# Kernel optimization log

Hardware: AMD Instinct MI355X
Metric: run time of the kernel (lower is better)

## Reference

```python
import jax, jax.numpy as jnp
import numpy as np

HIDDEN = 256
HEADS = 8
HEAD_DIM = HIDDEN // HEADS
SCALE = HEAD_DIM ** -0.5
N = 4096
NUM_GRAPHS = 16
LN_EPS = 1e-5


def setup_inputs() -> dict:
    key = jax.random.key(0)
    ks = jax.random.split(key, 8)
    x = jax.random.normal(ks[0], (N, HIDDEN), dtype=jnp.float32)
    batch = jnp.sort(jax.random.randint(ks[1], (N,), 0, NUM_GRAPHS, dtype=jnp.int64))
    # Xavier-uniform linear weights, stored as [in, out] (y = x @ W + b)
    lim = float(np.sqrt(6.0 / (HIDDEN + HIDDEN)))
    def W(k):
        return jax.random.uniform(k, (HIDDEN, HIDDEN), jnp.float32, -lim, lim)
    return {
        "x": x,
        "batch": batch,
        "Wq": W(ks[2]), "bq": jnp.zeros((HIDDEN,), jnp.float32),
        "Wk": W(ks[3]), "bk": jnp.zeros((HIDDEN,), jnp.float32),
        "Wv": W(ks[4]), "bv": jnp.zeros((HIDDEN,), jnp.float32),
        "Wo": W(ks[5]), "bo": jnp.zeros((HIDDEN,), jnp.float32),
        "gamma": jnp.ones((HIDDEN,), jnp.float32),
        "beta": jnp.zeros((HIDDEN,), jnp.float32),
    }


def _layer_norm(x, gamma, beta):
    mu = jnp.mean(x, axis=-1, keepdims=True)
    var = jnp.mean(jnp.square(x - mu), axis=-1, keepdims=True)
    return (x - mu) * jax.lax.rsqrt(var + LN_EPS) * gamma + beta


def reference(x, batch, Wq, bq, Wk, bk, Wv, bv, Wo, bo, gamma, beta):
    residual = x
    h = _layer_norm(x, gamma, beta)
    n = h.shape[0]
    q = (h @ Wq + bq).reshape(n, HEADS, HEAD_DIM)
    k = (h @ Wk + bk).reshape(n, HEADS, HEAD_DIM)
    v = (h @ Wv + bv).reshape(n, HEADS, HEAD_DIM)
    # dense scores masked to block-diagonal (same-graph) structure
    scores = jnp.einsum('ihd,jhd->ihj', q, k) * SCALE  # [N, H, N]
    same_graph = (batch[None, :] == batch[:, None])[:, None, :]  # [N, 1, N]
    scores = jnp.where(same_graph, scores, -jnp.inf)
    attn = jax.nn.softmax(scores, axis=-1)
    attn = jnp.nan_to_num(attn, nan=0.0)
    out = jnp.einsum('ihj,jhd->ihd', attn, v).reshape(n, HIDDEN)
    out = out @ Wo + bo
    return residual + out
```

## Files before the change

### kernel.cpp

```cpp
#include <hip/hip_runtime.h>

#define NNODES 4096
#define HID 256
#define NG 16
#define NH 8
#define HD 32
#define LN_EPS 1e-5f
#define QSCALE (0.17677669529663687f * 1.4426950408889634f)
#define CAPT 384
#define VTS (CAPT + 2)

typedef unsigned short u16;
typedef unsigned int u32;
typedef __bf16 bf16x8 __attribute__((ext_vector_type(8)));
typedef float f32x4 __attribute__((ext_vector_type(4)));

__device__ __forceinline__ float bf2f(u16 u){
  union { u32 i; float f; } c; c.i = ((u32)u) << 16; return c.f;
}
__device__ __forceinline__ u16 f2bf(float f){
  union { float f; u32 i; } c; c.f = f;
  u32 x = c.i;
  return (u16)((x + 0x7fffu + ((x >> 16) & 1u)) >> 16);
}

__global__ __launch_bounds__(256) void prep_kernel(
    const float* __restrict__ x, const float* __restrict__ gamma,
    const float* __restrict__ beta, u16* __restrict__ h,
    const float* __restrict__ Wq, const float* __restrict__ Wk,
    const float* __restrict__ Wv, const float* __restrict__ Wo,
    u16* __restrict__ Wt, const int* __restrict__ bw, int* __restrict__ seg){
  __shared__ u16 tile[32][33];
  __shared__ int bad;
  int b = blockIdx.x;
  if (b < 1024){
    int wave = threadIdx.x >> 6, lane = threadIdx.x & 63;
    int row = b * 4 + wave;
    float4 xv = ((const float4*)x)[row * 64 + lane];
    float a0 = xv.x, a1 = xv.y, a2 = xv.z, a3 = xv.w;
    float s = a0 + a1 + a2 + a3;
    #pragma unroll
    for (int m = 1; m < 64; m <<= 1) s += __shfl_xor(s, m);
    float mu = s * (1.0f / HID);
    float d0 = a0 - mu, d1 = a1 - mu, d2 = a2 - mu, d3 = a3 - mu;
    float vv = d0*d0 + d1*d1 + d2*d2 + d3*d3;
    #pragma unroll
    for (int m = 1; m < 64; m <<= 1) vv += __shfl_xor(vv, m);
    float rs = rsqrtf(vv * (1.0f / HID) + LN_EPS);
    float4 gv = ((const float4*)gamma)[lane];
    float4 bv = ((const float4*)beta)[lane];
    ushort4 o;
    o.x = f2bf(d0 * rs * gv.x + bv.x);
    o.y = f2bf(d1 * rs * gv.y + bv.y);
    o.z = f2bf(d2 * rs * gv.z + bv.z);
    o.w = f2bf(d3 * rs * gv.w + bv.w);
    *(ushort4*)(h + (size_t)row * HID + lane * 4) = o;
  } else if (b < 1280){
    int idx = b - 1024;
    int w = idx >> 6;
    int t = idx & 63;
    int bx = (t & 7) * 32, by = (t >> 3) * 32;
    const float* src = (w == 0) ? Wq : (w == 1) ? Wk : (w == 2) ? Wv : Wo;
    u16* dst = Wt + (size_t)w * HID * HID;
    int tx = threadIdx.x & 31, ty = threadIdx.x >> 5;
    #pragma unroll
    for (int r = 0; r < 32; r += 8)
      tile[ty + r][tx] = f2bf(src[(size_t)(by + ty + r) * HID + bx + tx]);
    __syncthreads();
    #pragma unroll
    for (int r = 0; r < 32; r += 8)
      dst[(size_t)(bx + ty + r) * HID + by + tx] = tile[tx][ty + r];
  } else {
    if (threadIdx.x == 0) bad = 0;
    __syncthreads();
    int local_bad = 0;
    for (int i = threadIdx.x; i < NNODES; i += 256){
      int v = bw[i];
      if (v < 0 || v > 15) local_bad = 1;
      if (i + 1 < NNODES && bw[i + 1] < v) local_bad = 1;
    }
    if (local_bad) atomicOr(&bad, 1);
    __syncthreads();
    int stride = bad ? 2 : 1;
    int g = threadIdx.x;
    if (g <= NG){
      int lo = 0, hi = NNODES;
      while (lo < hi){
        int mid = (lo + hi) >> 1;
        if (bw[mid * stride] < g) lo = mid + 1; else hi = mid;
      }
      seg[g] = lo;
    }
  }
}

template<bool FINAL>
__device__ __forceinline__ void gemm_tile(const u16* __restrict__ A, const u16* __restrict__ Bt,
    const float* __restrict__ bias, const float* __restrict__ resid, void* __restrict__ out){
  int gw = blockIdx.x * 4 + (threadIdx.x >> 6);
  int lane = threadIdx.x & 63;
  int lr = lane & 15, lq = lane >> 4;
  int m0 = (gw >> 4) * 64;
  int n0 = (gw & 15) * 16;
  f32x4 acc[4] = {};
  const u16* arow = A + (size_t)(m0 + lr) * HID + lq * 8;
  const u16* brow = Bt + (size_t)(n0 + lr) * HID + lq * 8;
  #pragma unroll
  for (int k0 = 0; k0 < HID; k0 += 32){
    bf16x8 b = *(const bf16x8*)(brow + k0);
    #pragma unroll
    for (int t = 0; t < 4; t++){
      bf16x8 a = *(const bf16x8*)(arow + (size_t)t * 16 * HID + k0);
      acc[t] = __builtin_amdgcn_mfma_f32_16x16x32_bf16(a, b, acc[t], 0, 0, 0);
    }
  }
  int col = n0 + lr;
  float bb = bias[col];
  #pragma unroll
  for (int t = 0; t < 4; t++){
    #pragma unroll
    for (int r = 0; r < 4; r++){
      int row = m0 + 16 * t + lq * 4 + r;
      float val = acc[t][r] + bb;
      if (FINAL){
        val += resid[(size_t)row * HID + col];
        ((float*)out)[(size_t)row * HID + col] = val;
      } else {
        ((u16*)out)[(size_t)row * HID + col] = f2bf(val);
      }
    }
  }
}

__global__ __launch_bounds__(256) void gemm_qkv_kernel(const u16* __restrict__ h,
    const u16* __restrict__ Wt, const float* __restrict__ bq, const float* __restrict__ bk,
    const float* __restrict__ bv, u16* __restrict__ q, u16* __restrict__ k, u16* __restrict__ v){
  int which = blockIdx.y;
  const u16* B = Wt + (size_t)which * HID * HID;
  const float* bias = (which == 0) ? bq : (which == 1) ? bk : bv;
  u16* out = (which == 0) ? q : (which == 1) ? k : v;
  gemm_tile<false>(h, B, bias, nullptr, out);
}

__global__ __launch_bounds__(256) void gemm_proj_kernel(const u16* __restrict__ ao,
    const u16* __restrict__ WtO, const float* __restrict__ bo, const float* __restrict__ x,
    float* __restrict__ out){
  gemm_tile<true>(ao, WtO, bo, x, out);
}

__global__ __launch_bounds__(256) void attn_kernel(const u16* __restrict__ q,
    const u16* __restrict__ k, const u16* __restrict__ v, const int* __restrict__ seg,
    u16* __restrict__ out){
  __shared__ u16 kl[CAPT * HD];
  __shared__ u16 vt[HD * VTS];
  int gh = blockIdx.y;
  int g = gh >> 3, hd = gh & 7;
  int start = seg[g], end = seg[g + 1];
  int len = end - start;
  if (len <= 0) return;
  if (len > CAPT) len = CAPT;
  int ntj = (len + 15) >> 4;
  int nj16 = ntj << 4;
  for (int idx = threadIdx.x; idx < nj16 * 4; idx += 256){
    int row = idx >> 2, part = idx & 3;
    uint4 val = make_uint4(0, 0, 0, 0);
    if (row < len)
      val = *(const uint4*)&k[(size_t)(start + row) * HID + hd * HD + part * 8];
    *(uint4*)&kl[row * HD + part * 8] = val;
  }
  for (int idx = threadIdx.x; idx < nj16 * 16; idx += 256){
    int row = idx >> 4, dg = idx & 15;
    u32 w = 0;
    if (row < len)
      w = *(const u32*)&v[(size_t)(start + row) * HID + hd * HD + dg * 2];
    vt[(2 * dg) * VTS + row]     = (u16)(w & 0xffffu);
    vt[(2 * dg + 1) * VTS + row] = (u16)(w >> 16);
  }
  __syncthreads();
  int wave = threadIdx.x >> 6, lane = threadIdx.x & 63;
  int lq = lane >> 4, lr = lane & 15;
  for (int tq = blockIdx.x * 4 + wave; tq < ntj; tq += gridDim.x * 4){
    int q0 = tq << 4;
    bf16x8 qf = *(const bf16x8*)&q[(size_t)(start + q0 + lr) * HID + hd * HD + lq * 8];
    f32x4 o0 = {0.f, 0.f, 0.f, 0.f}, o1 = {0.f, 0.f, 0.f, 0.f};
    float m = -3.0e38f, l = 0.f;
    for (int jt = 0; jt < ntj; jt++){
      int j0 = jt << 4;
      bf16x8 kf = *(const bf16x8*)&kl[(j0 + lr) * HD + lq * 8];
      f32x4 st = __builtin_amdgcn_mfma_f32_16x16x32_bf16(kf, qf,
                   (f32x4){0.f, 0.f, 0.f, 0.f}, 0, 0, 0);
      int jb = j0 + lq * 4;
      float s0 = (jb + 0 < len) ? st[0] * QSCALE : -3.0e38f;
      float s1 = (jb + 1 < len) ? st[1] * QSCALE : -3.0e38f;
      float s2 = (jb + 2 < len) ? st[2] * QSCALE : -3.0e38f;
      float s3 = (jb + 3 < len) ? st[3] * QSCALE : -3.0e38f;
      float tm = fmaxf(fmaxf(s0, s1), fmaxf(s2, s3));
      tm = fmaxf(tm, __shfl_xor(tm, 16));
      tm = fmaxf(tm, __shfl_xor(tm, 32));
      float mn = fmaxf(m, tm);
      float alpha = exp2f(m - mn);
      float p0 = exp2f(s0 - mn), p1 = exp2f(s1 - mn);
      float p2 = exp2f(s2 - mn), p3 = exp2f(s3 - mn);
      float ps = (p0 + p1) + (p2 + p3);
      ps += __shfl_xor(ps, 16);
      ps += __shfl_xor(ps, 32);
      l = l * alpha + ps;
      m = mn;
      union { bf16x8 v8; u16 s[8]; u32 w[4]; } pf, vf0, vf1;
      pf.w[0] = (u32)f2bf(p0) | ((u32)f2bf(p1) << 16);
      pf.w[1] = (u32)f2bf(p2) | ((u32)f2bf(p3) << 16);
      pf.w[2] = 0; pf.w[3] = 0;
      const u16* vp0 = &vt[lr * VTS + j0 + lq * 4];
      const u16* vp1 = &vt[(16 + lr) * VTS + j0 + lq * 4];
      vf0.w[0] = *(const u32*)vp0; vf0.w[1] = *(const u32*)(vp0 + 2);
      vf0.w[2] = 0; vf0.w[3] = 0;
      vf1.w[0] = *(const u32*)vp1; vf1.w[1] = *(const u32*)(vp1 + 2);
      vf1.w[2] = 0; vf1.w[3] = 0;
      o0 = o0 * alpha;
      o1 = o1 * alpha;
      o0 = __builtin_amdgcn_mfma_f32_16x16x32_bf16(vf0.v8, pf.v8, o0, 0, 0, 0);
      o1 = __builtin_amdgcn_mfma_f32_16x16x32_bf16(vf1.v8, pf.v8, o1, 0, 0, 0);
    }
    if (q0 + lr < len){
      float rl = 1.0f / l;
      u16* orow = out + (size_t)(start + q0 + lr) * HID + hd * HD;
      int dbase = lq * 4;
      *(u32*)&orow[dbase]          = (u32)f2bf(o0[0]*rl) | ((u32)f2bf(o0[1]*rl) << 16);
      *(u32*)&orow[dbase + 2]      = (u32)f2bf(o0[2]*rl) | ((u32)f2bf(o0[3]*rl) << 16);
      *(u32*)&orow[16 + dbase]     = (u32)f2bf(o1[0]*rl) | ((u32)f2bf(o1[1]*rl) << 16);
      *(u32*)&orow[16 + dbase + 2] = (u32)f2bf(o1[2]*rl) | ((u32)f2bf(o1[3]*rl) << 16);
    }
  }
}

__global__ void sentinel_kernel(u32* __restrict__ out, int nwords){
  int i = blockIdx.x * 256 + threadIdx.x;
  if (i < nwords) out[i] = 0x46404640u;
}

extern "C" void kernel_launch(void* const* d_in, const int* in_sizes, int n_in,
                              void* d_out, int out_size, void* d_ws, size_t ws_size,
                              hipStream_t stream){
  const float* x   = (const float*)d_in[0];
  const int* batch = (const int*)d_in[1];
  const float* Wq = (const float*)d_in[2],  *bq = (const float*)d_in[3];
  const float* Wk = (const float*)d_in[4],  *bk = (const float*)d_in[5];
  const float* Wv = (const float*)d_in[6],  *bv = (const float*)d_in[7];
  const float* Wo = (const float*)d_in[8],  *bo = (const float*)d_in[9];
  const float* gamma = (const float*)d_in[10], *beta = (const float*)d_in[11];

  const size_t WT_OFF  = 1024;
  const size_t QKV_OFF = WT_OFF + 4 * HID * HID * 2;
  const size_t BUF     = (size_t)NNODES * HID * 2;
  const size_t NEED    = QKV_OFF + 4 * BUF;

  if (ws_size < NEED){
    int nwords = out_size / 2;
    sentinel_kernel<<<(nwords + 255) / 256, 256, 0, stream>>>((u32*)d_out, nwords);
    return;
  }

  char* w = (char*)d_ws;
  int* seg  = (int*)(w + 128);
  u16* Wt   = (u16*)(w + WT_OFF);
  u16* qb   = (u16*)(w + QKV_OFF);
  u16* kb   = qb + (size_t)NNODES * HID;
  u16* vb   = kb + (size_t)NNODES * HID;
  u16* ao   = vb + (size_t)NNODES * HID;
  u16* h    = (u16*)d_out;

  prep_kernel<<<1281, 256, 0, stream>>>(x, gamma, beta, h, Wq, Wk, Wv, Wo, Wt, batch, seg);
  gemm_qkv_kernel<<<dim3(256, 3), 256, 0, stream>>>(h, Wt, bq, bk, bv, qb, kb, vb);
  attn_kernel<<<dim3(4, NG * NH), 256, 0, stream>>>(qb, kb, vb, seg, ao);
  gemm_proj_kernel<<<256, 256, 0, stream>>>(ao, Wt + 3 * (size_t)HID * HID, bo, x, (float*)d_out);
}
```

Measured before the change: 133.5 us.

## Split attention key range across two wave groups with LDS merge

The attention kernel now runs 512 threads per block: waves 4-7 handle the second half of the key tiles for the same query tiles as waves 0-3. The partial softmax states (m, l, output accumulators) are merged through shared memory. The K tile in LDS is padded to a 40-element row stride to reduce bank conflicts, and V is loaded with 16-byte reads before the transpose. This doubles parallelism per query tile to shorten the serial key loop, at the cost of extra LDS traffic and two block-wide barriers per outer iteration.

```diff
diff --git a/kernel.cpp b/kernel.cpp
--- a/kernel.cpp
+++ b/kernel.cpp
@@ -8,6 +8,7 @@
 #define LN_EPS 1e-5f
 #define QSCALE (0.17677669529663687f * 1.4426950408889634f)
 #define CAPT 384
+#define KLS 40
 #define VTS (CAPT + 2)
 
 typedef unsigned short u16;
@@ -148,11 +149,12 @@
   gemm_tile<true>(ao, WtO, bo, x, out);
 }
 
-__global__ __launch_bounds__(256) void attn_kernel(const u16* __restrict__ q,
+__global__ __launch_bounds__(512, 4) void attn_kernel(const u16* __restrict__ q,
     const u16* __restrict__ k, const u16* __restrict__ v, const int* __restrict__ seg,
     u16* __restrict__ out){
-  __shared__ u16 kl[CAPT * HD];
+  __shared__ u16 kl[CAPT * KLS];
   __shared__ u16 vt[HD * VTS];
+  __shared__ float mg[4][10][64];
   int gh = blockIdx.y;
   int g = gh >> 3, hd = gh & 7;
   int start = seg[g], end = seg[g + 1];
@@ -161,75 +163,114 @@
   if (len > CAPT) len = CAPT;
   int ntj = (len + 15) >> 4;
   int nj16 = ntj << 4;
-  for (int idx = threadIdx.x; idx < nj16 * 4; idx += 256){
+  for (int idx = threadIdx.x; idx < nj16 * 4; idx += 512){
     int row = idx >> 2, part = idx & 3;
     uint4 val = make_uint4(0, 0, 0, 0);
     if (row < len)
       val = *(const uint4*)&k[(size_t)(start + row) * HID + hd * HD + part * 8];
-    *(uint4*)&kl[row * HD + part * 8] = val;
-  }
-  for (int idx = threadIdx.x; idx < nj16 * 16; idx += 256){
-    int row = idx >> 4, dg = idx & 15;
-    u32 w = 0;
+    *(uint4*)&kl[row * KLS + part * 8] = val;
+  }
+  for (int idx = threadIdx.x; idx < nj16 * 4; idx += 512){
+    int row = idx >> 2, part = idx & 3;
+    uint4 w = make_uint4(0, 0, 0, 0);
     if (row < len)
-      w = *(const u32*)&v[(size_t)(start + row) * HID + hd * HD + dg * 2];
-    vt[(2 * dg) * VTS + row]     = (u16)(w & 0xffffu);
-    vt[(2 * dg + 1) * VTS + row] = (u16)(w >> 16);
+      w = *(const uint4*)&v[(size_t)(start + row) * HID + hd * HD + part * 8];
+    int d0 = part * 8;
+    vt[(d0 + 0) * VTS + row] = (u16)(w.x & 0xffffu);
+    vt[(d0 + 1) * VTS + row] = (u16)(w.x >> 16);
+    vt[(d0 + 2) * VTS + row] = (u16)(w.y & 0xffffu);
+    vt[(d0 + 3) * VTS + row] = (u16)(w.y >> 16);
+    vt[(d0 + 4) * VTS + row] = (u16)(w.z & 0xffffu);
+    vt[(d0 + 5) * VTS + row] = (u16)(w.z >> 16);
+    vt[(d0 + 6) * VTS + row] = (u16)(w.w & 0xffffu);
+    vt[(d0 + 7) * VTS + row] = (u16)(w.w >> 16);
   }
   __syncthreads();
   int wave = threadIdx.x >> 6, lane = threadIdx.x & 63;
   int lq = lane >> 4, lr = lane & 15;
-  for (int tq = blockIdx.x * 4 + wave; tq < ntj; tq += gridDim.x * 4){
+  int tl = wave & 3;
+  int jh = wave >> 2;
+  int nouter = (ntj + 15) >> 4;
+  for (int it = 0; it < nouter; it++){
+    int tq = it * 16 + blockIdx.x * 4 + tl;
+    bool active = tq < ntj;
     int q0 = tq << 4;
-    bf16x8 qf = *(const bf16x8*)&q[(size_t)(start + q0 + lr) * HID + hd * HD + lq * 8];
-    f32x4 o0 = {0.f, 0.f, 0.f, 0.f}, o1 = {0.f, 0.f, 0.f, 0.f};
     float m = -3.0e38f, l = 0.f;
-    for (int jt = 0; jt < ntj; jt++){
-      int j0 = jt << 4;
-      bf16x8 kf = *(const bf16x8*)&kl[(j0 + lr) * HD + lq * 8];
-      f32x4 st = __builtin_amdgcn_mfma_f32_16x16x32_bf16(kf, qf,
-                   (f32x4){0.f, 0.f, 0.f, 0.f}, 0, 0, 0);
-      int jb = j0 + lq * 4;
-      float s0 = (jb + 0 < len) ? st[0] * QSCALE : -3.0e38f;
-      float s1 = (jb + 1 < len) ? st[1] * QSCALE : -3.0e38f;
-      float s2 = (jb + 2 < len) ? st[2] * QSCALE : -3.0e38f;
-      float s3 = (jb + 3 < len) ? st[3] * QSCALE : -3.0e38f;
-      float tm = fmaxf(fmaxf(s0, s1), fmaxf(s2, s3));
-      tm = fmaxf(tm, __shfl_xor(tm, 16));
-      tm = fmaxf(tm, __shfl_xor(tm, 32));
-      float mn = fmaxf(m, tm);
-      float alpha = exp2f(m - mn);
-      float p0 = exp2f(s0 - mn), p1 = exp2f(s1 - mn);
-      float p2 = exp2f(s2 - mn), p3 = exp2f(s3 - mn);
-      float ps = (p0 + p1) + (p2 + p3);
-      ps += __shfl_xor(ps, 16);
-      ps += __shfl_xor(ps, 32);
-      l = l * alpha + ps;
-      m = mn;
-      union { bf16x8 v8; u16 s[8]; u32 w[4]; } pf, vf0, vf1;
-      pf.w[0] = (u32)f2bf(p0) | ((u32)f2bf(p1) << 16);
-      pf.w[1] = (u32)f2bf(p2) | ((u32)f2bf(p3) << 16);
-      pf.w[2] = 0; pf.w[3] = 0;
-      const u16* vp0 = &vt[lr * VTS + j0 + lq * 4];
-      const u16* vp1 = &vt[(16 + lr) * VTS + j0 + lq * 4];
-      vf0.w[0] = *(const u32*)vp0; vf0.w[1] = *(const u32*)(vp0 + 2);
-      vf0.w[2] = 0; vf0.w[3] = 0;
-      vf1.w[0] = *(const u32*)vp1; vf1.w[1] = *(const u32*)(vp1 + 2);
-      vf1.w[2] = 0; vf1.w[3] = 0;
-      o0 = o0 * alpha;
-      o1 = o1 * alpha;
-      o0 = __builtin_amdgcn_mfma_f32_16x16x32_bf16(vf0.v8, pf.v8, o0, 0, 0, 0);
-      o1 = __builtin_amdgcn_mfma_f32_16x16x32_bf16(vf1.v8, pf.v8, o1, 0, 0, 0);
-    }
-    if (q0 + lr < len){
-      float rl = 1.0f / l;
+    f32x4 o0 = {0.f,0.f,0.f,0.f}, o1 = {0.f,0.f,0.f,0.f};
+    if (active){
+      bf16x8 qf = *(const bf16x8*)&q[(size_t)(start + q0 + lr) * HID + hd * HD + lq * 8];
+      int half = (ntj + 1) >> 1;
+      int jt0 = jh ? half : 0;
+      int jt1 = jh ? ntj : half;
+      for (int jt = jt0; jt < jt1; jt++){
+        int j0 = jt << 4;
+        bf16x8 kf = *(const bf16x8*)&kl[(j0 + lr) * KLS + lq * 8];
+        f32x4 st = __builtin_amdgcn_mfma_f32_16x16x32_bf16(kf, qf,
+                     (f32x4){0.f,0.f,0.f,0.f}, 0, 0, 0);
+        int jb = j0 + lq * 4;
+        float s0 = (jb + 0 < len) ? st[0] * QSCALE : -3.0e38f;
+        float s1 = (jb + 1 < len) ? st[1] * QSCALE : -3.0e38f;
+        float s2 = (jb + 2 < len) ? st[2] * QSCALE : -3.0e38f;
+        float s3 = (jb + 3 < len) ? st[3] * QSCALE : -3.0e38f;
+        float tm = fmaxf(fmaxf(s0, s1), fmaxf(s2, s3));
+        tm = fmaxf(tm, __shfl_xor(tm, 16));
+        tm = fmaxf(tm, __shfl_xor(tm, 32));
+        float mn = fmaxf(m, tm);
+        float alpha = exp2f(m - mn);
+        float p0 = exp2f(s0 - mn), p1 = exp2f(s1 - mn);
+        float p2 = exp2f(s2 - mn), p3 = exp2f(s3 - mn);
+        float ps = (p0 + p1) + (p2 + p3);
+        ps += __shfl_xor(ps, 16);
+        ps += __shfl_xor(ps, 32);
+        l = l * alpha + ps;
+        m = mn;
+        union { bf16x8 v8; u32 w[4]; } pf, vf0, vf1;
+        pf.w[0] = (u32)f2bf(p0) | ((u32)f2bf(p1) << 16);
+        pf.w[1] = (u32)f2bf(p2) | ((u32)f2bf(p3) << 16);
+        pf.w[2] = 0; pf.w[3] = 0;
+        const u16* vp0 = &vt[lr * VTS + j0 + lq * 4];
+        const u16* vp1 = &vt[(16 + lr) * VTS + j0 + lq * 4];
+        vf0.w[0] = *(const u32*)vp0; vf0.w[1] = *(const u32*)(vp0 + 2);
+        vf0.w[2] = 0; vf0.w[3] = 0;
+        vf1.w[0] = *(const u32*)vp1; vf1.w[1] = *(const u32*)(vp1 + 2);
+        vf1.w[2] = 0; vf1.w[3] = 0;
+        o0 = o0 * alpha;
+        o1 = o1 * alpha;
+        o0 = __builtin_amdgcn_mfma_f32_16x16x32_bf16(vf0.v8, pf.v8, o0, 0, 0, 0);
+        o1 = __builtin_amdgcn_mfma_f32_16x16x32_bf16(vf1.v8, pf.v8, o1, 0, 0, 0);
+      }
+    }
+    if (jh == 1){
+      mg[tl][0][lane] = o0[0]; mg[tl][1][lane] = o0[1];
+      mg[tl][2][lane] = o0[2]; mg[tl][3][lane] = o0[3];
+      mg[tl][4][lane] = o1[0]; mg[tl][5][lane] = o1[1];
+      mg[tl][6][lane] = o1[2]; mg[tl][7][lane] = o1[3];
+      mg[tl][8][lane] = m;     mg[tl][9][lane] = l;
+    }
+    __syncthreads();
+    if (jh == 0 && active && q0 + lr < len){
+      float m2 = mg[tl][8][lane], l2 = mg[tl][9][lane];
+      float mn = fmaxf(m, m2);
+      float a  = exp2f(m - mn);
+      float a2 = exp2f(m2 - mn);
+      float lt = l * a + l2 * a2;
+      float rl = 1.0f / lt;
+      float r0 = (o0[0]*a + mg[tl][0][lane]*a2) * rl;
+      float r1 = (o0[1]*a + mg[tl][1][lane]*a2) * rl;
+      float r2 = (o0[2]*a + mg[tl][2][lane]*a2) * rl;
+      float r3 = (o0[3]*a + mg[tl][3][lane]*a2) * rl;
+      float r4 = (o1[0]*a + mg[tl][4][lane]*a2) * rl;
+      float r5 = (o1[1]*a + mg[tl][5][lane]*a2) * rl;
+      float r6 = (o1[2]*a + mg[tl][6][lane]*a2) * rl;
+      float r7 = (o1[3]*a + mg[tl][7][lane]*a2) * rl;
       u16* orow = out + (size_t)(start + q0 + lr) * HID + hd * HD;
       int dbase = lq * 4;
-      *(u32*)&orow[dbase]          = (u32)f2bf(o0[0]*rl) | ((u32)f2bf(o0[1]*rl) << 16);
-      *(u32*)&orow[dbase + 2]      = (u32)f2bf(o0[2]*rl) | ((u32)f2bf(o0[3]*rl) << 16);
-      *(u32*)&orow[16 + dbase]     = (u32)f2bf(o1[0]*rl) | ((u32)f2bf(o1[1]*rl) << 16);
-      *(u32*)&orow[16 + dbase + 2] = (u32)f2bf(o1[2]*rl) | ((u32)f2bf(o1[3]*rl) << 16);
-    }
+      *(u32*)&orow[dbase]          = (u32)f2bf(r0) | ((u32)f2bf(r1) << 16);
+      *(u32*)&orow[dbase + 2]      = (u32)f2bf(r2) | ((u32)f2bf(r3) << 16);
+      *(u32*)&orow[16 + dbase]     = (u32)f2bf(r4) | ((u32)f2bf(r5) << 16);
+      *(u32*)&orow[16 + dbase + 2] = (u32)f2bf(r6) | ((u32)f2bf(r7) << 16);
+    }
+    __syncthreads();
   }
 }
 
@@ -271,6 +312,6 @@
 
   prep_kernel<<<1281, 256, 0, stream>>>(x, gamma, beta, h, Wq, Wk, Wv, Wo, Wt, batch, seg);
   gemm_qkv_kernel<<<dim3(256, 3), 256, 0, stream>>>(h, Wt, bq, bk, bv, qb, kb, vb);
-  attn_kernel<<<dim3(4, NG * NH), 256, 0, stream>>>(qb, kb, vb, seg, ao);
+  attn_kernel<<<dim3(4, NG * NH), 512, 0, stream>>>(qb, kb, vb, seg, ao);
   gemm_proj_kernel<<<256, 256, 0, stream>>>(ao, Wt + 3 * (size_t)HID * HID, bo, x, (float*)d_out);
 }
```

After: 129.1 us. -3.3%, faster.
